# Kernel optimization log

Hardware: AMD Instinct MI355X
Metric: run time of the kernel (lower is better)

Reference implementation:

```python
import jax, jax.numpy as jnp
import numpy as np

B, S, HID = 2, 2048, 2048
N_HEADS = 16
HEAD_DIM = HID // N_HEADS  # 128
ROPE_THETA = 10000.0
MAX_SEQ = 4096


def _rope_cache(position_ids, head_dim, theta=ROPE_THETA, max_seq=MAX_SEQ):
    # standard RoPE cache: cos/sin of shape [B, S, head_dim//2]
    half = head_dim // 2
    inv_freq = 1.0 / theta ** (jnp.arange(half, dtype=jnp.float32) / half)
    t = jnp.arange(max_seq, dtype=jnp.float32)
    freqs = jnp.outer(t, inv_freq)                      # [max_seq, half]
    pos = jnp.clip(position_ids, 0, max_seq - 1)
    return jnp.cos(freqs)[pos], jnp.sin(freqs)[pos]     # [B, S, half]


def _apply_rope(q, k, cos, sin):
    # q,k: [B, H, S, D]; cos/sin: [B, S, D/2] -> [B, 1, S, D/2]
    cos = cos[:, None, :, :]
    sin = sin[:, None, :, :]
    q1, q2 = jnp.split(q, 2, axis=-1)
    k1, k2 = jnp.split(k, 2, axis=-1)
    q_rot = jnp.concatenate([q1 * cos - q2 * sin, q2 * cos + q1 * sin], axis=-1)
    k_rot = jnp.concatenate([k1 * cos - k2 * sin, k2 * cos + k1 * sin], axis=-1)
    return q_rot, k_rot


def setup_inputs() -> dict:
    key = jax.random.key(0)
    ks = jax.random.split(key, 6)
    hidden_states = jax.random.normal(ks[0], (B, S, HID), dtype=jnp.float32)
    # additive causal mask, broadcastable over batch and heads
    causal = jnp.tril(jnp.ones((S, S), dtype=bool))
    attention_mask = jnp.where(causal, 0.0, -1e9).astype(jnp.float32)[None, None]
    position_ids = jnp.broadcast_to(jnp.arange(S, dtype=jnp.int32)[None, :], (B, S))
    scale = 0.02
    Wq = jax.random.normal(ks[1], (HID, N_HEADS * HEAD_DIM), dtype=jnp.float32) * scale
    Wk = jax.random.normal(ks[2], (HID, N_HEADS * HEAD_DIM), dtype=jnp.float32) * scale
    Wv = jax.random.normal(ks[3], (HID, N_HEADS * HEAD_DIM), dtype=jnp.float32) * scale
    Wo = jax.random.normal(ks[4], (N_HEADS * HEAD_DIM, HID), dtype=jnp.float32) * scale
    zeros = jnp.zeros((HID,), dtype=jnp.float32)
    return {
        "hidden_states": hidden_states,
        "attention_mask": attention_mask,
        "position_ids": position_ids,
        "Wq": Wq, "bq": zeros,
        "Wk": Wk, "bk": zeros,
        "Wv": Wv, "bv": zeros,
        "Wo": Wo, "bo": zeros,
    }


def reference(hidden_states, attention_mask, position_ids,
              Wq, bq, Wk, bk, Wv, bv, Wo, bo):
    b, s, _ = hidden_states.shape
    q = (hidden_states @ Wq + bq).reshape(b, s, N_HEADS, HEAD_DIM).transpose(0, 2, 1, 3)
    k = (hidden_states @ Wk + bk).reshape(b, s, N_HEADS, HEAD_DIM).transpose(0, 2, 1, 3)
    v = (hidden_states @ Wv + bv).reshape(b, s, N_HEADS, HEAD_DIM).transpose(0, 2, 1, 3)

    cos, sin = _rope_cache(position_ids, HEAD_DIM)
    q, k = _apply_rope(q, k, cos, sin)

    scores = jnp.einsum("bhqd,bhkd->bhqk", q, k) / jnp.sqrt(jnp.float32(HEAD_DIM))
    scores = scores + attention_mask
    weights = jax.nn.softmax(scores, axis=-1)
    attn = jnp.einsum("bhqk,bhkd->bhqd", weights, v)  # [B,H,S,D]
    attn = attn.transpose(0, 2, 1, 3).reshape(b, s, N_HEADS * HEAD_DIM)
    return attn @ Wo + bo
```

## Files before the change

### kernel.cpp

```cpp
#include <hip/hip_runtime.h>
#include <hip/hip_bf16.h>

typedef __bf16 bf16;
typedef bf16 bf16x4 __attribute__((ext_vector_type(4)));
typedef bf16 bf16x8 __attribute__((ext_vector_type(8)));
typedef float f32x4 __attribute__((ext_vector_type(4)));

#define B_ 2
#define S_ 2048
#define HID_ 2048
#define NH_ 16
#define HD_ 128
#define M_TOT (B_ * S_)
#define RSCALE 0.08838834764831845f
#define LN10000_OVER_64 0.14391156f

#define OFF_XB   0ull
#define OFF_WQT  (OFF_XB  + (size_t)M_TOT*HID_*2)
#define OFF_WKT  (OFF_WQT + (size_t)HID_*HID_*2)
#define OFF_WVT  (OFF_WKT + (size_t)HID_*HID_*2)
#define OFF_WOT  (OFF_WVT + (size_t)HID_*HID_*2)
#define OFF_QB   (OFF_WOT + (size_t)HID_*HID_*2)
#define OFF_KB   (OFF_QB  + (size_t)M_TOT*HID_*2)
#define OFF_VTB  (OFF_KB  + (size_t)M_TOT*HID_*2)
#define OFF_AB   (OFF_VTB + (size_t)M_TOT*HID_*2)

__global__ __launch_bounds__(256) void cvt_x(const float* __restrict__ x,
                                             bf16* __restrict__ o) {
    size_t i = ((size_t)blockIdx.x * 256 + threadIdx.x) * 4;
    float4 v = *(const float4*)(x + i);
    bf16x4 r; r[0] = (bf16)v.x; r[1] = (bf16)v.y; r[2] = (bf16)v.z; r[3] = (bf16)v.w;
    *(bf16x4*)(o + i) = r;
}

__global__ __launch_bounds__(256) void trans_w(const float* w0, const float* w1,
                                               const float* w2, const float* w3,
                                               bf16* o0, bf16* o1, bf16* o2, bf16* o3) {
    const float* W; bf16* O;
    switch (blockIdx.z) {
        case 0: W = w0; O = o0; break;
        case 1: W = w1; O = o1; break;
        case 2: W = w2; O = o2; break;
        default: W = w3; O = o3; break;
    }
    __shared__ float t[64][65];
    int tid = threadIdx.x;
    int nt0 = blockIdx.x * 64, kt0 = blockIdx.y * 64;
    #pragma unroll
    for (int p = 0; p < 4; ++p) {
        int r = p * 16 + (tid >> 4);
        int c = (tid & 15) * 4;
        float4 v = *(const float4*)(W + (size_t)(kt0 + r) * HID_ + nt0 + c);
        t[r][c + 0] = v.x; t[r][c + 1] = v.y; t[r][c + 2] = v.z; t[r][c + 3] = v.w;
    }
    __syncthreads();
    #pragma unroll
    for (int p = 0; p < 4; ++p) {
        int rr = p * 16 + (tid >> 4);
        int cc = (tid & 15) * 4;
        bf16x4 v;
        v[0] = (bf16)t[cc + 0][rr]; v[1] = (bf16)t[cc + 1][rr];
        v[2] = (bf16)t[cc + 2][rr]; v[3] = (bf16)t[cc + 3][rr];
        *(bf16x4*)(O + (size_t)(nt0 + rr) * HID_ + kt0 + cc) = v;
    }
}

template <int MODE>
__global__ __launch_bounds__(256) void gemm_k(const bf16* __restrict__ A,
                                              const bf16* __restrict__ Bt,
                                              const float* __restrict__ bias,
                                              const int* __restrict__ pos_ids,
                                              void* __restrict__ out) {
    __shared__ bf16 Al[128][72];
    __shared__ bf16 Bl[128][72];
    const int tid = threadIdx.x;
    const int l = tid & 63, w = tid >> 6;
    const int ln = l & 15, lg = l >> 4;
    const int bm = blockIdx.y, bn = blockIdx.x;

    f32x4 acc[2][8] = {};

    for (int k0 = 0; k0 < HID_; k0 += 64) {
        #pragma unroll
        for (int p = 0; p < 4; ++p) {
            int r = p * 32 + (tid >> 3);
            int c8 = (tid & 7) * 8;
            *(uint4*)&Al[r][c8] = *(const uint4*)(A  + (size_t)(bm * 128 + r) * HID_ + k0 + c8);
            *(uint4*)&Bl[r][c8] = *(const uint4*)(Bt + (size_t)(bn * 128 + r) * HID_ + k0 + c8);
        }
        __syncthreads();
        #pragma unroll
        for (int kk = 0; kk < 2; ++kk) {
            bf16x8 af[2], bfv[8];
            #pragma unroll
            for (int fm = 0; fm < 2; ++fm)
                af[fm] = *(const bf16x8*)&Al[w * 32 + fm * 16 + ln][kk * 32 + lg * 8];
            #pragma unroll
            for (int fn = 0; fn < 8; ++fn)
                bfv[fn] = *(const bf16x8*)&Bl[fn * 16 + ln][kk * 32 + lg * 8];
            #pragma unroll
            for (int fm = 0; fm < 2; ++fm)
                #pragma unroll
                for (int fn = 0; fn < 8; ++fn)
                    acc[fm][fn] = __builtin_amdgcn_mfma_f32_16x16x32_bf16(
                        af[fm], bfv[fn], acc[fm][fn], 0, 0, 0);
        }
        __syncthreads();
    }

    #pragma unroll
    for (int fm = 0; fm < 2; ++fm) {
        #pragma unroll
        for (int i = 0; i < 4; ++i) {
            int m_g = bm * 128 + w * 32 + fm * 16 + lg * 4 + i;
            if (MODE == 3) {
                float* O = (float*)out;
                #pragma unroll
                for (int fn = 0; fn < 8; ++fn) {
                    int n_g = bn * 128 + fn * 16 + ln;
                    O[(size_t)m_g * HID_ + n_g] = acc[fm][fn][i] + bias[n_g];
                }
            } else if (MODE == 2) {
                int b = m_g >> 11, s = m_g & (S_ - 1);
                bf16* O = (bf16*)out;
                #pragma unroll
                for (int fn = 0; fn < 8; ++fn) {
                    int d = fn * 16 + ln;
                    float v = acc[fm][fn][i] + bias[bn * 128 + d];
                    O[((size_t)(b * NH_ + bn) * HD_ + d) * S_ + s] = (bf16)v;
                }
            } else {
                int b = m_g >> 11, s = m_g & (S_ - 1);
                int pos = pos_ids[m_g];
                pos = pos < 0 ? 0 : (pos > 4095 ? 4095 : pos);
                size_t base = ((size_t)(b * NH_ + bn) * S_ + s) * HD_;
                bf16* O = (bf16*)out;
                #pragma unroll
                for (int fn = 0; fn < 4; ++fn) {
                    int j = fn * 16 + ln;
                    float x1 = acc[fm][fn][i]     + bias[bn * 128 + j];
                    float x2 = acc[fm][fn + 4][i] + bias[bn * 128 + j + 64];
                    float invf = __expf(-(float)j * LN10000_OVER_64);
                    float ang = (float)pos * invf;
                    float sn, cs;
                    __sincosf(ang, &sn, &cs);
                    float y1 = x1 * cs - x2 * sn;
                    float y2 = x2 * cs + x1 * sn;
                    if (MODE == 0) { y1 *= RSCALE; y2 *= RSCALE; }
                    O[base + j]      = (bf16)y1;
                    O[base + j + 64] = (bf16)y2;
                }
            }
        }
    }
}

__global__ __launch_bounds__(256) void attn_k(const bf16* __restrict__ Q,
                                              const bf16* __restrict__ K,
                                              const bf16* __restrict__ Vt,
                                              bf16* __restrict__ O) {
    __shared__ bf16 Kl[64][136];
    __shared__ bf16 Vl[128][72];
    __shared__ bf16 Pl[4][16][72];
    const int tid = threadIdx.x;
    const int l = tid & 63, w = tid >> 6;
    const int ln = l & 15, lg = l >> 4;
    const int qt = blockIdx.x, bh = blockIdx.y;

    const bf16* Qb = Q  + (size_t)bh * S_ * HD_;
    const bf16* Kb = K  + (size_t)bh * S_ * HD_;
    const bf16* Vb = Vt + (size_t)bh * S_ * HD_;

    const int qrow = qt * 64 + w * 16 + ln;
    bf16x8 qf[4];
    #pragma unroll
    for (int kk = 0; kk < 4; ++kk)
        qf[kk] = *(const bf16x8*)(Qb + (size_t)qrow * HD_ + kk * 32 + lg * 8);

    float m_run[4], l_run[4];
    #pragma unroll
    for (int i = 0; i < 4; ++i) { m_run[i] = -1e30f; l_run[i] = 0.f; }
    f32x4 oacc[8] = {};

    const int qg0 = qt * 64 + w * 16 + lg * 4;

    for (int kt = 0; kt <= qt; ++kt) {
        #pragma unroll
        for (int p = 0; p < 4; ++p) {
            int r = p * 16 + (tid >> 4), c8 = (tid & 15) * 8;
            *(uint4*)&Kl[r][c8] = *(const uint4*)(Kb + (size_t)(kt * 64 + r) * HD_ + c8);
        }
        #pragma unroll
        for (int p = 0; p < 4; ++p) {
            int r = p * 32 + (tid >> 3), c8 = (tid & 7) * 8;
            *(uint4*)&Vl[r][c8] = *(const uint4*)(Vb + (size_t)r * S_ + kt * 64 + c8);
        }
        __syncthreads();

        f32x4 sacc[4] = {};
        #pragma unroll
        for (int kk = 0; kk < 4; ++kk) {
            bf16x8 kf[4];
            #pragma unroll
            for (int n = 0; n < 4; ++n)
                kf[n] = *(const bf16x8*)&Kl[n * 16 + ln][kk * 32 + lg * 8];
            #pragma unroll
            for (int n = 0; n < 4; ++n)
                sacc[n] = __builtin_amdgcn_mfma_f32_16x16x32_bf16(qf[kk], kf[n], sacc[n], 0, 0, 0);
        }

        if (kt == qt) {
            #pragma unroll
            for (int n = 0; n < 4; ++n)
                #pragma unroll
                for (int i = 0; i < 4; ++i) {
                    int kg = kt * 64 + n * 16 + ln;
                    if (kg > qg0 + i) sacc[n][i] = -1e30f;
                }
        }

        float mt[4];
        #pragma unroll
        for (int i = 0; i < 4; ++i) {
            mt[i] = fmaxf(fmaxf(sacc[0][i], sacc[1][i]), fmaxf(sacc[2][i], sacc[3][i]));
            #pragma unroll
            for (int d = 1; d < 16; d <<= 1)
                mt[i] = fmaxf(mt[i], __shfl_xor(mt[i], d));
        }
        float scale[4], rs[4];
        #pragma unroll
        for (int i = 0; i < 4; ++i) {
            float mnew = fmaxf(m_run[i], mt[i]);
            scale[i] = __expf(m_run[i] - mnew);
            m_run[i] = mnew;
            rs[i] = 0.f;
        }
        #pragma unroll
        for (int n = 0; n < 4; ++n)
            #pragma unroll
            for (int i = 0; i < 4; ++i) {
                float p = __expf(sacc[n][i] - m_run[i]);
                sacc[n][i] = p;
                rs[i] += p;
            }
        #pragma unroll
        for (int i = 0; i < 4; ++i) {
            #pragma unroll
            for (int d = 1; d < 16; d <<= 1)
                rs[i] += __shfl_xor(rs[i], d);
            l_run[i] = l_run[i] * scale[i] + rs[i];
        }
        #pragma unroll
        for (int dn = 0; dn < 8; ++dn)
            #pragma unroll
            for (int i = 0; i < 4; ++i)
                oacc[dn][i] *= scale[i];

        #pragma unroll
        for (int n = 0; n < 4; ++n)
            #pragma unroll
            for (int i = 0; i < 4; ++i)
                Pl[w][lg * 4 + i][n * 16 + ln] = (bf16)sacc[n][i];
        __syncthreads();

        #pragma unroll
        for (int kk = 0; kk < 2; ++kk) {
            bf16x8 pf = *(const bf16x8*)&Pl[w][ln][kk * 32 + lg * 8];
            #pragma unroll
            for (int dn = 0; dn < 8; ++dn) {
                bf16x8 vf = *(const bf16x8*)&Vl[dn * 16 + ln][kk * 32 + lg * 8];
                oacc[dn] = __builtin_amdgcn_mfma_f32_16x16x32_bf16(pf, vf, oacc[dn], 0, 0, 0);
            }
        }
        __syncthreads();
    }

    const int b = bh >> 4, h = bh & (NH_ - 1);
    #pragma unroll
    for (int i = 0; i < 4; ++i) {
        float inv = 1.0f / l_run[i];
        int s = qt * 64 + w * 16 + lg * 4 + i;
        #pragma unroll
        for (int dn = 0; dn < 8; ++dn) {
            int d = dn * 16 + ln;
            O[((size_t)(b * S_ + s)) * HID_ + h * HD_ + d] = (bf16)(oacc[dn][i] * inv);
        }
    }
}

extern "C" void kernel_launch(void* const* d_in, const int* in_sizes, int n_in,
                              void* d_out, int out_size, void* d_ws, size_t ws_size,
                              hipStream_t stream) {
    const float* X    = (const float*)d_in[0];
    const int*   pos  = (const int*)d_in[2];
    const float* Wq   = (const float*)d_in[3];
    const float* bq   = (const float*)d_in[4];
    const float* Wk   = (const float*)d_in[5];
    const float* bk   = (const float*)d_in[6];
    const float* Wv   = (const float*)d_in[7];
    const float* bv   = (const float*)d_in[8];
    const float* Wo   = (const float*)d_in[9];
    const float* bo   = (const float*)d_in[10];
    float* Out = (float*)d_out;

    char* ws = (char*)d_ws;
    bf16* Xb  = (bf16*)(ws + OFF_XB);
    bf16* Wqt = (bf16*)(ws + OFF_WQT);
    bf16* Wkt = (bf16*)(ws + OFF_WKT);
    bf16* Wvt = (bf16*)(ws + OFF_WVT);
    bf16* Wot = (bf16*)(ws + OFF_WOT);
    bf16* Qb  = (bf16*)(ws + OFF_QB);
    bf16* Kb  = (bf16*)(ws + OFF_KB);
    bf16* Vtb = (bf16*)(ws + OFF_VTB);
    bf16* Ab  = (bf16*)(ws + OFF_AB);

    cvt_x<<<(M_TOT * HID_) / (256 * 4), 256, 0, stream>>>(X, Xb);
    trans_w<<<dim3(32, 32, 4), 256, 0, stream>>>(Wq, Wk, Wv, Wo, Wqt, Wkt, Wvt, Wot);

    dim3 gg(HID_ / 128, M_TOT / 128);
    gemm_k<0><<<gg, 256, 0, stream>>>(Xb, Wqt, bq, pos, (void*)Qb);
    gemm_k<1><<<gg, 256, 0, stream>>>(Xb, Wkt, bk, pos, (void*)Kb);
    gemm_k<2><<<gg, 256, 0, stream>>>(Xb, Wvt, bv, pos, (void*)Vtb);

    attn_k<<<dim3(S_ / 64, B_ * NH_), 256, 0, stream>>>(Qb, Kb, Vtb, Ab);

    gemm_k<3><<<gg, 256, 0, stream>>>(Ab, Wot, bo, pos, (void*)Out);
}
```

Before: 390.2 us.

## Load-balance causal attention with paired tiles and prefetch; direct-to-LDS GEMM loads

Attention now uses 512-thread blocks covering 128 query rows. Each block handles two query tiles, j and 15-j, so every block does a similar amount of causal work. The next K/V tile is prefetched into registers while the current one is processed, and the per-wave barrier before the P·V step is dropped. The GEMM stages A/B tiles with global_load_lds straight into LDS, which requires unpadded 64-column rows and may bring back LDS bank conflicts on the fragment reads. The barrier placement is also rearranged so there is one sync at the top of each k-step.

```diff
diff --git a/kernel.cpp b/kernel.cpp
--- a/kernel.cpp
+++ b/kernel.cpp
@@ -25,6 +25,12 @@
 #define OFF_VTB  (OFF_KB  + (size_t)M_TOT*HID_*2)
 #define OFF_AB   (OFF_VTB + (size_t)M_TOT*HID_*2)
 
+__device__ __forceinline__ void gload16(const bf16* g, bf16* l) {
+    typedef const __attribute__((address_space(1))) unsigned int gu32;
+    typedef __attribute__((address_space(3))) unsigned int lu32;
+    __builtin_amdgcn_global_load_lds((gu32*)g, (lu32*)l, 16, 0, 0);
+}
+
 __global__ __launch_bounds__(256) void cvt_x(const float* __restrict__ x,
                                              bf16* __restrict__ o) {
     size_t i = ((size_t)blockIdx.x * 256 + threadIdx.x) * 4;
@@ -71,8 +77,8 @@
                                               const float* __restrict__ bias,
                                               const int* __restrict__ pos_ids,
                                               void* __restrict__ out) {
-    __shared__ bf16 Al[128][72];
-    __shared__ bf16 Bl[128][72];
+    __shared__ bf16 Al[128][64];
+    __shared__ bf16 Bl[128][64];
     const int tid = threadIdx.x;
     const int l = tid & 63, w = tid >> 6;
     const int ln = l & 15, lg = l >> 4;
@@ -81,12 +87,14 @@
     f32x4 acc[2][8] = {};
 
     for (int k0 = 0; k0 < HID_; k0 += 64) {
-        #pragma unroll
-        for (int p = 0; p < 4; ++p) {
-            int r = p * 32 + (tid >> 3);
-            int c8 = (tid & 7) * 8;
-            *(uint4*)&Al[r][c8] = *(const uint4*)(A  + (size_t)(bm * 128 + r) * HID_ + k0 + c8);
-            *(uint4*)&Bl[r][c8] = *(const uint4*)(Bt + (size_t)(bn * 128 + r) * HID_ + k0 + c8);
+        __syncthreads();
+        #pragma unroll
+        for (int j = 0; j < 4; ++j) {
+            int r0 = w * 32 + j * 8;
+            int r = r0 + (l >> 3);
+            int c = (l & 7) * 8;
+            gload16(A  + (size_t)(bm * 128 + r) * HID_ + k0 + c, &Al[r0][0]);
+            gload16(Bt + (size_t)(bn * 128 + r) * HID_ + k0 + c, &Bl[r0][0]);
         }
         __syncthreads();
         #pragma unroll
@@ -105,7 +113,6 @@
                     acc[fm][fn] = __builtin_amdgcn_mfma_f32_16x16x32_bf16(
                         af[fm], bfv[fn], acc[fm][fn], 0, 0, 0);
         }
-        __syncthreads();
     }
 
     #pragma unroll
@@ -155,135 +162,151 @@
     }
 }
 
-__global__ __launch_bounds__(256) void attn_k(const bf16* __restrict__ Q,
+__global__ __launch_bounds__(512) void attn_k(const bf16* __restrict__ Q,
                                               const bf16* __restrict__ K,
                                               const bf16* __restrict__ Vt,
                                               bf16* __restrict__ O) {
     __shared__ bf16 Kl[64][136];
     __shared__ bf16 Vl[128][72];
-    __shared__ bf16 Pl[4][16][72];
+    __shared__ bf16 Pl[8][16][72];
     const int tid = threadIdx.x;
     const int l = tid & 63, w = tid >> 6;
     const int ln = l & 15, lg = l >> 4;
-    const int qt = blockIdx.x, bh = blockIdx.y;
+    const int pair = blockIdx.x, bh = blockIdx.y;
 
     const bf16* Qb = Q  + (size_t)bh * S_ * HD_;
     const bf16* Kb = K  + (size_t)bh * S_ * HD_;
     const bf16* Vb = Vt + (size_t)bh * S_ * HD_;
-
-    const int qrow = qt * 64 + w * 16 + ln;
-    bf16x8 qf[4];
-    #pragma unroll
-    for (int kk = 0; kk < 4; ++kk)
-        qf[kk] = *(const bf16x8*)(Qb + (size_t)qrow * HD_ + kk * 32 + lg * 8);
-
-    float m_run[4], l_run[4];
-    #pragma unroll
-    for (int i = 0; i < 4; ++i) { m_run[i] = -1e30f; l_run[i] = 0.f; }
-    f32x4 oacc[8] = {};
-
-    const int qg0 = qt * 64 + w * 16 + lg * 4;
-
-    for (int kt = 0; kt <= qt; ++kt) {
-        #pragma unroll
-        for (int p = 0; p < 4; ++p) {
-            int r = p * 16 + (tid >> 4), c8 = (tid & 15) * 8;
-            *(uint4*)&Kl[r][c8] = *(const uint4*)(Kb + (size_t)(kt * 64 + r) * HD_ + c8);
-        }
-        #pragma unroll
-        for (int p = 0; p < 4; ++p) {
-            int r = p * 32 + (tid >> 3), c8 = (tid & 7) * 8;
-            *(uint4*)&Vl[r][c8] = *(const uint4*)(Vb + (size_t)r * S_ + kt * 64 + c8);
-        }
-        __syncthreads();
-
-        f32x4 sacc[4] = {};
-        #pragma unroll
-        for (int kk = 0; kk < 4; ++kk) {
-            bf16x8 kf[4];
+    const int b = bh >> 4, h = bh & (NH_ - 1);
+
+    uint4 kr[2], vr[2];
+
+    for (int rep = 0; rep < 2; ++rep) {
+        const int j = rep ? (15 - pair) : pair;
+        const int nkt = 2 * j + 2;
+        const int qrow = j * 128 + w * 16 + ln;
+        const int qg0  = j * 128 + w * 16 + lg * 4;
+
+        bf16x8 qf[4];
+        #pragma unroll
+        for (int kk = 0; kk < 4; ++kk)
+            qf[kk] = *(const bf16x8*)(Qb + (size_t)qrow * HD_ + kk * 32 + lg * 8);
+
+        float m_run[4], l_run[4];
+        #pragma unroll
+        for (int i = 0; i < 4; ++i) { m_run[i] = -1e30f; l_run[i] = 0.f; }
+        f32x4 oacc[8] = {};
+
+        #pragma unroll
+        for (int m = 0; m < 2; ++m) {
+            int f = m * 512 + tid;
+            kr[m] = *(const uint4*)(Kb + (size_t)(f >> 4) * HD_ + (f & 15) * 8);
+            vr[m] = *(const uint4*)(Vb + (size_t)(f >> 3) * S_ + (f & 7) * 8);
+        }
+
+        for (int kt = 0; kt < nkt; ++kt) {
+            __syncthreads();
+            #pragma unroll
+            for (int m = 0; m < 2; ++m) {
+                int f = m * 512 + tid;
+                *(uint4*)&Kl[f >> 4][(f & 15) * 8] = kr[m];
+                *(uint4*)&Vl[f >> 3][(f & 7) * 8] = vr[m];
+            }
+            __syncthreads();
+            if (kt + 1 < nkt) {
+                #pragma unroll
+                for (int m = 0; m < 2; ++m) {
+                    int f = m * 512 + tid;
+                    kr[m] = *(const uint4*)(Kb + (size_t)((kt + 1) * 64 + (f >> 4)) * HD_ + (f & 15) * 8);
+                    vr[m] = *(const uint4*)(Vb + (size_t)(f >> 3) * S_ + (kt + 1) * 64 + (f & 7) * 8);
+                }
+            }
+
+            f32x4 sacc[4] = {};
+            #pragma unroll
+            for (int kk = 0; kk < 4; ++kk) {
+                bf16x8 kf[4];
+                #pragma unroll
+                for (int n = 0; n < 4; ++n)
+                    kf[n] = *(const bf16x8*)&Kl[n * 16 + ln][kk * 32 + lg * 8];
+                #pragma unroll
+                for (int n = 0; n < 4; ++n)
+                    sacc[n] = __builtin_amdgcn_mfma_f32_16x16x32_bf16(qf[kk], kf[n], sacc[n], 0, 0, 0);
+            }
+
+            if (kt >= 2 * j) {
+                #pragma unroll
+                for (int n = 0; n < 4; ++n)
+                    #pragma unroll
+                    for (int i = 0; i < 4; ++i) {
+                        int kg = kt * 64 + n * 16 + ln;
+                        if (kg > qg0 + i) sacc[n][i] = -1e30f;
+                    }
+            }
+
+            float mt[4];
+            #pragma unroll
+            for (int i = 0; i < 4; ++i) {
+                mt[i] = fmaxf(fmaxf(sacc[0][i], sacc[1][i]), fmaxf(sacc[2][i], sacc[3][i]));
+                #pragma unroll
+                for (int d = 1; d < 16; d <<= 1)
+                    mt[i] = fmaxf(mt[i], __shfl_xor(mt[i], d));
+            }
+            float scale[4], rs[4];
+            #pragma unroll
+            for (int i = 0; i < 4; ++i) {
+                float mnew = fmaxf(m_run[i], mt[i]);
+                scale[i] = __expf(m_run[i] - mnew);
+                m_run[i] = mnew;
+                rs[i] = 0.f;
+            }
             #pragma unroll
             for (int n = 0; n < 4; ++n)
-                kf[n] = *(const bf16x8*)&Kl[n * 16 + ln][kk * 32 + lg * 8];
+                #pragma unroll
+                for (int i = 0; i < 4; ++i) {
+                    float p = __expf(sacc[n][i] - m_run[i]);
+                    sacc[n][i] = p;
+                    rs[i] += p;
+                }
+            #pragma unroll
+            for (int i = 0; i < 4; ++i) {
+                #pragma unroll
+                for (int d = 1; d < 16; d <<= 1)
+                    rs[i] += __shfl_xor(rs[i], d);
+                l_run[i] = l_run[i] * scale[i] + rs[i];
+            }
+            #pragma unroll
+            for (int dn = 0; dn < 8; ++dn)
+                #pragma unroll
+                for (int i = 0; i < 4; ++i)
+                    oacc[dn][i] *= scale[i];
+
             #pragma unroll
             for (int n = 0; n < 4; ++n)
-                sacc[n] = __builtin_amdgcn_mfma_f32_16x16x32_bf16(qf[kk], kf[n], sacc[n], 0, 0, 0);
-        }
-
-        if (kt == qt) {
-            #pragma unroll
-            for (int n = 0; n < 4; ++n)
-                #pragma unroll
-                for (int i = 0; i < 4; ++i) {
-                    int kg = kt * 64 + n * 16 + ln;
-                    if (kg > qg0 + i) sacc[n][i] = -1e30f;
-                }
-        }
-
-        float mt[4];
+                #pragma unroll
+                for (int i = 0; i < 4; ++i)
+                    Pl[w][lg * 4 + i][n * 16 + ln] = (bf16)sacc[n][i];
+
+            #pragma unroll
+            for (int kk = 0; kk < 2; ++kk) {
+                bf16x8 pf = *(const bf16x8*)&Pl[w][ln][kk * 32 + lg * 8];
+                #pragma unroll
+                for (int dn = 0; dn < 8; ++dn) {
+                    bf16x8 vf = *(const bf16x8*)&Vl[dn * 16 + ln][kk * 32 + lg * 8];
+                    oacc[dn] = __builtin_amdgcn_mfma_f32_16x16x32_bf16(pf, vf, oacc[dn], 0, 0, 0);
+                }
+            }
+        }
+
         #pragma unroll
         for (int i = 0; i < 4; ++i) {
-            mt[i] = fmaxf(fmaxf(sacc[0][i], sacc[1][i]), fmaxf(sacc[2][i], sacc[3][i]));
-            #pragma unroll
-            for (int d = 1; d < 16; d <<= 1)
-                mt[i] = fmaxf(mt[i], __shfl_xor(mt[i], d));
-        }
-        float scale[4], rs[4];
-        #pragma unroll
-        for (int i = 0; i < 4; ++i) {
-            float mnew = fmaxf(m_run[i], mt[i]);
-            scale[i] = __expf(m_run[i] - mnew);
-            m_run[i] = mnew;
-            rs[i] = 0.f;
-        }
-        #pragma unroll
-        for (int n = 0; n < 4; ++n)
-            #pragma unroll
-            for (int i = 0; i < 4; ++i) {
-                float p = __expf(sacc[n][i] - m_run[i]);
-                sacc[n][i] = p;
-                rs[i] += p;
-            }
-        #pragma unroll
-        for (int i = 0; i < 4; ++i) {
-            #pragma unroll
-            for (int d = 1; d < 16; d <<= 1)
-                rs[i] += __shfl_xor(rs[i], d);
-            l_run[i] = l_run[i] * scale[i] + rs[i];
-        }
-        #pragma unroll
-        for (int dn = 0; dn < 8; ++dn)
-            #pragma unroll
-            for (int i = 0; i < 4; ++i)
-                oacc[dn][i] *= scale[i];
-
-        #pragma unroll
-        for (int n = 0; n < 4; ++n)
-            #pragma unroll
-            for (int i = 0; i < 4; ++i)
-                Pl[w][lg * 4 + i][n * 16 + ln] = (bf16)sacc[n][i];
-        __syncthreads();
-
-        #pragma unroll
-        for (int kk = 0; kk < 2; ++kk) {
-            bf16x8 pf = *(const bf16x8*)&Pl[w][ln][kk * 32 + lg * 8];
+            float inv = 1.0f / l_run[i];
+            int s = j * 128 + w * 16 + lg * 4 + i;
             #pragma unroll
             for (int dn = 0; dn < 8; ++dn) {
-                bf16x8 vf = *(const bf16x8*)&Vl[dn * 16 + ln][kk * 32 + lg * 8];
-                oacc[dn] = __builtin_amdgcn_mfma_f32_16x16x32_bf16(pf, vf, oacc[dn], 0, 0, 0);
-            }
-        }
-        __syncthreads();
-    }
-
-    const int b = bh >> 4, h = bh & (NH_ - 1);
-    #pragma unroll
-    for (int i = 0; i < 4; ++i) {
-        float inv = 1.0f / l_run[i];
-        int s = qt * 64 + w * 16 + lg * 4 + i;
-        #pragma unroll
-        for (int dn = 0; dn < 8; ++dn) {
-            int d = dn * 16 + ln;
-            O[((size_t)(b * S_ + s)) * HID_ + h * HD_ + d] = (bf16)(oacc[dn][i] * inv);
+                int d = dn * 16 + ln;
+                O[((size_t)(b * S_ + s)) * HID_ + h * HD_ + d] = (bf16)(oacc[dn][i] * inv);
+            }
         }
     }
 }
@@ -322,7 +345,7 @@
     gemm_k<1><<<gg, 256, 0, stream>>>(Xb, Wkt, bk, pos, (void*)Kb);
     gemm_k<2><<<gg, 256, 0, stream>>>(Xb, Wvt, bv, pos, (void*)Vtb);
 
-    attn_k<<<dim3(S_ / 64, B_ * NH_), 256, 0, stream>>>(Qb, Kb, Vtb, Ab);
+    attn_k<<<dim3(8, B_ * NH_), 512, 0, stream>>>(Qb, Kb, Vtb, Ab);
 
     gemm_k<3><<<gg, 256, 0, stream>>>(Ab, Wot, bo, pos, (void*)Out);
 }
```

After: 367.4 us. 1.06x faster.
